# Kernel tuning notes

Hardware: AMD Instinct MI355X
Metric: run time of the kernel (lower is better)

The kernel has to match this reference:

```python
import jax, jax.numpy as jnp
import numpy as np

T, B, H = 2048, 8, 16
KF, VF, KS, VS = 32, 64, 128, 64


def _l2norm(x, eps=1e-6):
    return x / jnp.sqrt(jnp.sum(x * x, axis=-1, keepdims=True) + eps)


def setup_inputs() -> dict:
    key = jax.random.key(0)
    ks = jax.random.split(key, 12)
    # k/q are L2-normalized externally (per E88/E90 kernel contract)
    k_fast = _l2norm(jax.random.normal(ks[0], (T, B, H, KF), jnp.float32))
    q_fast = _l2norm(jax.random.normal(ks[1], (T, B, H, KF), jnp.float32))
    v_fast = jax.random.normal(ks[2], (T, B, H, VF), jnp.float32)
    k_slow = _l2norm(jax.random.normal(ks[3], (T, B, H, KS), jnp.float32))
    q_slow = _l2norm(jax.random.normal(ks[4], (T, B, H, KS), jnp.float32))
    v_slow = jax.random.normal(ks[5], (T, B, H, VS), jnp.float32)
    # decay factors in (0.85, 1.0): typical Mamba2-style per-head scalar decay
    decay_fast = 0.85 + 0.15 * jax.random.uniform(ks[6], (T, B, H), jnp.float32)
    decay_slow = 0.85 + 0.15 * jax.random.uniform(ks[7], (T, B, H), jnp.float32)
    slow_gate = jax.random.uniform(ks[8], (T, B, H), jnp.float32)
    mix_fast = jax.random.uniform(ks[9], (T, B, H), jnp.float32)
    mix_slow = jax.random.uniform(ks[10], (T, B, H), jnp.float32)
    S_fast0 = jnp.zeros((B, H, KF, VF), jnp.float32)
    S_slow0 = jnp.zeros((B, H, KS, VS), jnp.float32)
    return dict(k_fast=k_fast, v_fast=v_fast, q_fast=q_fast, decay_fast=decay_fast,
                k_slow=k_slow, v_slow=v_slow, q_slow=q_slow, decay_slow=decay_slow,
                slow_gate=slow_gate, mix_fast=mix_fast, mix_slow=mix_slow,
                S_fast0=S_fast0, S_slow0=S_slow0, n_heads=H)


def _e90_scan(k_fast, v_fast, q_fast, decay_fast,
              k_slow, v_slow, q_slow, decay_slow,
              slow_gate, mix_fast, mix_slow, S_fast0, S_slow0):
    def step(carry, x):
        S_f, S_s = carry  # [B,H,KF,VF], [B,H,KS,VS]
        kf, vf, qf, df, ksl, vsl, qsl, dsl, g, mf, ms = x
        # fast state: updated every timestep (decay + rank-1 outer product)
        S_f = df[..., None, None] * S_f + kf[..., :, None] * vf[..., None, :]
        # slow state: gated soft update
        S_s_new = dsl[..., None, None] * S_s + ksl[..., :, None] * vsl[..., None, :]
        g_ = g[..., None, None]
        S_s = g_ * S_s_new + (1.0 - g_) * S_s
        out_f = jnp.einsum('bhk,bhkv->bhv', qf, S_f)
        out_s = jnp.einsum('bhk,bhkv->bhv', qsl, S_s)
        out = mf[..., None] * out_f + ms[..., None] * out_s
        return (S_f, S_s), out

    xs = (k_fast, v_fast, q_fast, decay_fast,
          k_slow, v_slow, q_slow, decay_slow,
          slow_gate, mix_fast, mix_slow)
    (S_f_final, S_s_final), output = jax.lax.scan(step, (S_fast0, S_slow0), xs)
    return S_f_final, S_s_final, output  # output: [T,B,H,VF]


def reference(k_fast, v_fast, q_fast, decay_fast, k_slow, v_slow, q_slow,
              decay_slow, slow_gate, mix_fast, mix_slow, S_fast0, S_slow0, n_heads):
    return _e90_scan(k_fast, v_fast, q_fast, decay_fast,
                     k_slow, v_slow, q_slow, decay_slow,
                     slow_gate, mix_fast, mix_slow, S_fast0, S_slow0)
```

## Files before the change

### kernel.cpp

```cpp
#include <hip/hip_runtime.h>

#define T_STEPS 2048
#define BH      128
#define KS_     128
#define VS_     64
#define KF_     32
#define VF_     64
#define LCH     32
#define NC      (T_STEPS / LCH)
#define NTHR    512

typedef __attribute__((ext_vector_type(8))) short short8;
typedef __attribute__((ext_vector_type(16))) float f32x16;

#define MFMA32(a,b,c) __builtin_amdgcn_mfma_f32_32x32x16_bf16((a),(b),(c),0,0,0)
#define CROW(r,hi) (((r)&3) + 8*((r)>>2) + 4*(hi))

__device__ __forceinline__ unsigned short f2b(float x) {
    union { float f; unsigned u; } v; v.f = x;
    unsigned r = v.u + 0x7FFFu + ((v.u >> 16) & 1u);
    return (unsigned short)(r >> 16);
}
__device__ __forceinline__ unsigned cvtpk(float lo, float hi_) {
    unsigned r;
    asm("v_cvt_pk_bf16_f32 %0, %1, %2" : "=v"(r) : "v"(lo), "v"(hi_));
    return r;
}
__device__ __forceinline__ short8 ld8(const unsigned short* p) {
    return *(const short8*)p;
}

__global__ __launch_bounds__(NTHR, 2)
void e90_mfma(const float* __restrict__ k_fast,  const float* __restrict__ v_fast,
              const float* __restrict__ q_fast,  const float* __restrict__ decay_fast,
              const float* __restrict__ k_slow,  const float* __restrict__ v_slow,
              const float* __restrict__ q_slow,  const float* __restrict__ decay_slow,
              const float* __restrict__ slow_gate, const float* __restrict__ mix_fast,
              const float* __restrict__ mix_slow, const float* __restrict__ S_fast0,
              const float* __restrict__ S_slow0, float* __restrict__ dout)
{
    __shared__ __align__(16) unsigned short Qs  [2][LCH][136];
    __shared__ __align__(16) unsigned short Ksl [2][LCH][136];
    __shared__ __align__(16) unsigned short Sbs [2][LCH][136];
    __shared__ __align__(16) unsigned short Psl [2][LCH][40];
    __shared__ __align__(16) unsigned short Pfl [2][LCH][40];
    __shared__ __align__(16) unsigned short Qfl [2][LCH][40];
    __shared__ __align__(16) unsigned short Kfl [2][LCH][40];
    __shared__ __align__(16) unsigned short Sbfl[2][LCH][40];
    __shared__ __align__(16) unsigned short VTs [3][LCH][40];
    __shared__ __align__(16) unsigned short VTf [3][LCH][40];

    const int tid  = threadIdx.x;
    const int bid  = blockIdx.x;
    const int xcd  = bid & 7;
    const int jj   = bid >> 3;
    const int p    = xcd * 16 + (jj >> 1);
    const int v0   = (jj & 1) * 32;
    const int lane = tid & 63;
    const int wid  = tid >> 6;
    const int l31  = lane & 31;
    const int hi   = lane >> 5;
    const int s_   = tid >> 4;
    const int j0_  = (tid & 15) * 2;
    const int k0_  = (tid & 15) * 8;

    float* out_y = dout + BH*KF_*VF_ + BH*KS_*VS_;

    f32x16 Sst, oacc;
#pragma unroll
    for (int r = 0; r < 16; ++r) { Sst[r] = 0.0f; oacc[r] = 0.0f; }
    if (wid < 4) {
#pragma unroll
        for (int r = 0; r < 16; ++r)
            Sst[r] = S_slow0[((size_t)p*KS_ + 32*wid + CROW(r,hi))*VS_ + v0 + l31];
#pragma unroll
        for (int r = 0; r < 16; ++r) Sbs[0][l31][32*wid + CROW(r,hi)] = f2b(Sst[r]);
    } else if (wid == 4) {
#pragma unroll
        for (int r = 0; r < 16; ++r)
            Sst[r] = S_fast0[((size_t)p*KF_ + CROW(r,hi))*VF_ + v0 + l31];
#pragma unroll
        for (int r = 0; r < 16; ++r) Sbfl[0][l31][CROW(r,hi)] = f2b(Sst[r]);
    }

    float4 pKs0, pKs1, pQs0, pQs1;
    float2 pVs, pVf, pKf, pQf;
    float pL0 = 0.f, pL1 = 0.f, pL2 = 0.f;
    float bls = 1.f, blf = 1.f, ib = 1.f, ibf = 1.f, qsc = 0.f, qfc = 0.f, g_s = 0.f;

#define LOADVEC(CIDX) do {                                                     \
    int tc_ = (CIDX); if (tc_ > NC-1) tc_ = NC-1;                              \
    const int tb_ = tc_ * LCH;                                                 \
    const float* bk_ = k_slow + ((size_t)(tb_+s_)*BH + p)*KS_ + k0_;           \
    pKs0 = *(const float4*)bk_;  pKs1 = *(const float4*)(bk_+4);               \
    const float* bq_ = q_slow + ((size_t)(tb_+s_)*BH + p)*KS_ + k0_;           \
    pQs0 = *(const float4*)bq_;  pQs1 = *(const float4*)(bq_+4);               \
    pVs = *(const float2*)(v_slow + ((size_t)(tb_+s_)*BH + p)*VS_ + v0 + j0_); \
    pVf = *(const float2*)(v_fast + ((size_t)(tb_+s_)*BH + p)*VF_ + v0 + j0_); \
    pKf = *(const float2*)(k_fast + ((size_t)(tb_+s_)*BH + p)*KF_ + j0_);      \
    pQf = *(const float2*)(q_fast + ((size_t)(tb_+s_)*BH + p)*KF_ + j0_);      \
    } while (0)

#define LOADSCL(CIDX) do {                                                     \
    int tc_ = (CIDX); if (tc_ > NC-1) tc_ = NC-1;                              \
    const size_t so_ = (size_t)(tc_*LCH + l31)*BH + p;                         \
    pL0 = (hi ? decay_fast : decay_slow)[so_];                                 \
    pL1 = (hi ? mix_fast   : slow_gate )[so_];                                 \
    pL2 = hi ? 0.0f : mix_slow[so_];                                           \
    } while (0)

#define SCAN() do {                                                            \
    float a_ = hi ? pL0 : __builtin_fmaf(pL1, pL0, 1.0f - pL1);                \
    float b_ = a_;                                                             \
    _Pragma("unroll")                                                          \
    for (int d = 1; d < 32; d <<= 1) {                                         \
        float y_ = __shfl_up(b_, d, 32);                                       \
        if (l31 >= d) b_ *= y_;                                                \
    }                                                                          \
    float bs_s = __shfl(b_, s_);                                               \
    float bf_s = __shfl(b_, 32 + s_);                                          \
    bls = __shfl(b_, 31);                                                      \
    blf = __shfl(b_, 63);                                                      \
    g_s = __shfl(pL1, s_);                                                     \
    float mf_s = __shfl(pL1, 32 + s_);                                         \
    float ms_s = __shfl(pL2, s_);                                              \
    ib  = 1.0f / bs_s;                                                         \
    ibf = 1.0f / bf_s;                                                         \
    qsc = ms_s * bs_s;                                                         \
    qfc = mf_s * bf_s;                                                         \
    } while (0)

#define STAGE(J2, J3) do {                                                     \
    uint4 kw, qw;                                                              \
    kw.x = cvtpk(pKs0.x*ib, pKs0.y*ib);  kw.y = cvtpk(pKs0.z*ib, pKs0.w*ib);   \
    kw.z = cvtpk(pKs1.x*ib, pKs1.y*ib);  kw.w = cvtpk(pKs1.z*ib, pKs1.w*ib);   \
    qw.x = cvtpk(pQs0.x*qsc, pQs0.y*qsc); qw.y = cvtpk(pQs0.z*qsc, pQs0.w*qsc);\
    qw.z = cvtpk(pQs1.x*qsc, pQs1.y*qsc); qw.w = cvtpk(pQs1.z*qsc, pQs1.w*qsc);\
    *(uint4*)&Ksl[J2][s_][k0_] = kw;                                           \
    *(uint4*)&Qs [J2][s_][k0_] = qw;                                           \
    float vt0 = g_s*pVs.x, vt1 = g_s*pVs.y;                                    \
    VTs[J3][j0_  ][s_] = f2b(vt0);                                             \
    VTs[J3][j0_+1][s_] = f2b(vt1);                                             \
    VTf[J3][j0_  ][s_] = f2b(pVf.x);                                           \
    VTf[J3][j0_+1][s_] = f2b(pVf.y);                                           \
    unsigned kfp = cvtpk(pKf.x*ibf, pKf.y*ibf);                                \
    *(unsigned*)&Kfl[J2][s_][j0_] = kfp;                                       \
    unsigned qfp = cvtpk(pQf.x*qfc, pQf.y*qfc);                                \
    *(unsigned*)&Qfl[J2][s_][j0_] = qfp;                                       \
    } while (0)

#define YSTORE(CP) do {                                                        \
    const int p2_ = (CP) & 1, p3_ = (CP) % 3;                                  \
    f32x16 o2;                                                                 \
    _Pragma("unroll")                                                          \
    for (int r = 0; r < 16; ++r) o2[r] = 0.0f;                                 \
    const unsigned short* ar = &Psl[p2_][l31][0];                              \
    const unsigned short* br = &VTs[p3_][l31][0];                              \
    oacc = MFMA32(ld8(ar + 8*hi),      ld8(br + 8*hi),      oacc);             \
    oacc = MFMA32(ld8(ar + 16 + 8*hi), ld8(br + 16 + 8*hi), oacc);             \
    const unsigned short* af = &Pfl[p2_][l31][0];                              \
    const unsigned short* bf = &VTf[p3_][l31][0];                              \
    o2 = MFMA32(ld8(af + 8*hi),      ld8(bf + 8*hi),      o2);                 \
    o2 = MFMA32(ld8(af + 16 + 8*hi), ld8(bf + 16 + 8*hi), o2);                 \
    _Pragma("unroll")                                                          \
    for (int r = 0; r < 16; ++r) {                                             \
        int tr = CROW(r,hi);                                                   \
        out_y[((size_t)((CP)*LCH + tr)*BH + p)*VF_ + v0 + l31] = oacc[r] + o2[r]; \
    }                                                                          \
    } while (0)

    LOADVEC(0);
    LOADSCL(0);
    SCAN();
    LOADSCL(1);
    STAGE(0, 0);
    __syncthreads();

    for (int c = 0; c < NC; ++c) {
        const int i2 = c & 1;
        const int i3 = c % 3;

        LOADVEC(c + 1);

        if (wid < 4) {
            short8 a1, a2;
#pragma unroll
            for (int e = 0; e < 8; ++e) {
                a1[e] = (short)Ksl[i2][8*hi + e][32*wid + l31];
                a2[e] = (short)Ksl[i2][16 + 8*hi + e][32*wid + l31];
            }
            const unsigned short* br = &VTs[i3][l31][0];
            Sst = MFMA32(a1, ld8(br + 8*hi),      Sst);
            Sst = MFMA32(a2, ld8(br + 16 + 8*hi), Sst);
#pragma unroll
            for (int r = 0; r < 16; ++r) Sst[r] *= bls;
        } else if (wid == 4) {
            short8 a1, a2;
#pragma unroll
            for (int e = 0; e < 8; ++e) {
                a1[e] = (short)Kfl[i2][8*hi + e][l31];
                a2[e] = (short)Kfl[i2][16 + 8*hi + e][l31];
            }
            const unsigned short* br = &VTf[i3][l31][0];
            Sst = MFMA32(a1, ld8(br + 8*hi),      Sst);
            Sst = MFMA32(a2, ld8(br + 16 + 8*hi), Sst);
#pragma unroll
            for (int r = 0; r < 16; ++r) Sst[r] *= blf;
        } else if (wid == 5) {
            f32x16 p1, p2;
#pragma unroll
            for (int r = 0; r < 16; ++r) { p1[r] = 0.0f; p2[r] = 0.0f; }
            const unsigned short* ar = &Qs [i2][l31][0];
            const unsigned short* br = &Ksl[i2][l31][0];
            const int kb = 8*hi;
#pragma unroll
            for (int st = 0; st < 8; st += 2) {
                p1 = MFMA32(ld8(ar + kb + 16*st),     ld8(br + kb + 16*st),     p1);
                p2 = MFMA32(ld8(ar + kb + 16*(st+1)), ld8(br + kb + 16*(st+1)), p2);
            }
#pragma unroll
            for (int r = 0; r < 16; ++r) {
                int tr = CROW(r,hi);
                Psl[i2][tr][l31] = f2b(tr >= l31 ? p1[r] + p2[r] : 0.0f);
            }
        } else if (wid == 6) {
            f32x16 p1;
#pragma unroll
            for (int r = 0; r < 16; ++r) p1[r] = 0.0f;
            const unsigned short* ar = &Qfl[i2][l31][0];
            const unsigned short* br = &Kfl[i2][l31][0];
            p1 = MFMA32(ld8(ar + 8*hi),      ld8(br + 8*hi),      p1);
            p1 = MFMA32(ld8(ar + 16 + 8*hi), ld8(br + 16 + 8*hi), p1);
#pragma unroll
            for (int r = 0; r < 16; ++r) {
                int tr = CROW(r,hi);
                Pfl[i2][tr][l31] = f2b(tr >= l31 ? p1[r] : 0.0f);
            }
        } else {
            if (c > 0) YSTORE(c - 1);
            f32x16 o1, o2;
#pragma unroll
            for (int r = 0; r < 16; ++r) { o1[r] = 0.0f; o2[r] = 0.0f; }
            const unsigned short* ar = &Qs [i2][l31][0];
            const unsigned short* br = &Sbs[i2][l31][0];
            const int kb = 8*hi;
#pragma unroll
            for (int st = 0; st < 8; st += 2) {
                o1 = MFMA32(ld8(ar + kb + 16*st),     ld8(br + kb + 16*st),     o1);
                o2 = MFMA32(ld8(ar + kb + 16*(st+1)), ld8(br + kb + 16*(st+1)), o2);
            }
            const unsigned short* af = &Qfl [i2][l31][0];
            const unsigned short* bf = &Sbfl[i2][l31][0];
            o1 = MFMA32(ld8(af + 8*hi),      ld8(bf + 8*hi),      o1);
            o2 = MFMA32(ld8(af + 16 + 8*hi), ld8(bf + 16 + 8*hi), o2);
#pragma unroll
            for (int r = 0; r < 16; ++r) oacc[r] = o1[r] + o2[r];
        }

        SCAN();
        LOADSCL(c + 2);

        if (c < NC - 1) {
            const int j2 = (c + 1) & 1;
            const int j3 = (c + 1) % 3;
            if (wid < 4) {
#pragma unroll
                for (int r = 0; r < 16; ++r) Sbs[j2][l31][32*wid + CROW(r,hi)] = f2b(Sst[r]);
            } else if (wid == 4) {
#pragma unroll
                for (int r = 0; r < 16; ++r) Sbfl[j2][l31][CROW(r,hi)] = f2b(Sst[r]);
            }
            STAGE(j2, j3);
        }
        __syncthreads();
    }

    if (wid == 7) {
        YSTORE(NC - 1);
    }
    if (wid < 4) {
#pragma unroll
        for (int r = 0; r < 16; ++r)
            dout[BH*KF_*VF_ + ((size_t)p*KS_ + 32*wid + CROW(r,hi))*VS_ + v0 + l31] = Sst[r];
    } else if (wid == 4) {
#pragma unroll
        for (int r = 0; r < 16; ++r)
            dout[((size_t)p*KF_ + CROW(r,hi))*VF_ + v0 + l31] = Sst[r];
    }
#undef LOADVEC
#undef LOADSCL
#undef SCAN
#undef STAGE
#undef YSTORE
}

extern "C" void kernel_launch(void* const* d_in, const int* in_sizes, int n_in,
                              void* d_out, int out_size, void* d_ws, size_t ws_size,
                              hipStream_t stream)
{
    const float* k_fast     = (const float*)d_in[0];
    const float* v_fast     = (const float*)d_in[1];
    const float* q_fast     = (const float*)d_in[2];
    const float* decay_fast = (const float*)d_in[3];
    const float* k_slow     = (const float*)d_in[4];
    const float* v_slow     = (const float*)d_in[5];
    const float* q_slow     = (const float*)d_in[6];
    const float* decay_slow = (const float*)d_in[7];
    const float* slow_gate  = (const float*)d_in[8];
    const float* mix_fast   = (const float*)d_in[9];
    const float* mix_slow   = (const float*)d_in[10];
    const float* S_fast0    = (const float*)d_in[11];
    const float* S_slow0    = (const float*)d_in[12];
    float* dout = (float*)d_out;

    e90_mfma<<<dim3(256), dim3(NTHR), 0, stream>>>(
        k_fast, v_fast, q_fast, decay_fast,
        k_slow, v_slow, q_slow, decay_slow,
        slow_gate, mix_fast, mix_slow, S_fast0, S_slow0, dout);
}
```

Measured before the change: 186.9 us.

## Split sequence into two halves scanned in parallel with a state-correction kernel

Splits the time axis into two halves so each head/value slice runs two blocks, 512 in total instead of 256. The second half starts from zero state and records per-step cumulative decay scales and its local final state in a workspace. A second fix-up kernel then combines the first half's final state with those scales, adding q·S0 contributions to second-half outputs and correcting the final states. The aim is to double the parallelism of a latency-bound sequential scan, at the cost of an extra launch, workspace traffic, and dropping the multi-stage pipelining of the original loop.

```diff
diff --git a/kernel.cpp b/kernel.cpp
--- a/kernel.cpp
+++ b/kernel.cpp
@@ -7,8 +7,17 @@
 #define KF_     32
 #define VF_     64
 #define LCH     32
+#define NCG     32
 #define NC      (T_STEPS / LCH)
+#define HALF_T  1024
 #define NTHR    512
+#define WSLOT   5120
+#define SCLS_OFF 1310720
+#define SCLF_OFF 1835008
+#define RUN_OFF  2359296
+#define WS_NEEDED_BYTES ((size_t)(RUN_OFF + 512) * 4)
+#define SOFF    (BH*KF_*VF_)
+#define YOFF    (BH*KF_*VF_ + BH*KS_*VS_)
 
 typedef __attribute__((ext_vector_type(8))) short short8;
 typedef __attribute__((ext_vector_type(16))) float f32x16;
@@ -30,8 +39,390 @@
     return *(const short8*)p;
 }
 
+__global__ __launch_bounds__(NTHR, 4)
+void e90_scan(const float* __restrict__ k_fast,  const float* __restrict__ v_fast,
+              const float* __restrict__ q_fast,  const float* __restrict__ decay_fast,
+              const float* __restrict__ k_slow,  const float* __restrict__ v_slow,
+              const float* __restrict__ q_slow,  const float* __restrict__ decay_slow,
+              const float* __restrict__ slow_gate, const float* __restrict__ mix_fast,
+              const float* __restrict__ mix_slow, const float* __restrict__ S_fast0,
+              const float* __restrict__ S_slow0, float* __restrict__ dout,
+              float* __restrict__ dws)
+{
+    __shared__ __align__(16) unsigned short Qs [LCH][136];
+    __shared__ __align__(16) unsigned short Ksl[LCH][136];
+    __shared__ __align__(16) unsigned short Sbs[LCH][136];
+    __shared__ __align__(16) unsigned short Psl[LCH][40];
+    __shared__ __align__(16) unsigned short Pfl[LCH][40];
+    __shared__ __align__(16) unsigned short Qfl[LCH][40];
+    __shared__ __align__(16) unsigned short Kfl[LCH][40];
+    __shared__ __align__(16) unsigned short Sbfl[LCH][40];
+    __shared__ __align__(16) unsigned short VTs[2][LCH][40];
+    __shared__ __align__(16) unsigned short VTf[2][LCH][40];
+
+    const int tid  = threadIdx.x;
+    const int bid  = blockIdx.x;
+    const int xcd  = bid & 7;
+    const int q8   = bid >> 3;
+    const int p    = xcd * 16 + (q8 >> 2);
+    const int vh   = (q8 >> 1) & 1;
+    const int v0   = vh * 32;
+    const int th   = q8 & 1;
+    const int tgb  = th * HALF_T;
+    const int slot = p * 2 + vh;
+    const int lane = tid & 63;
+    const int wid  = tid >> 6;
+    const int l31  = lane & 31;
+    const int hi   = lane >> 5;
+    const int s_   = tid >> 4;
+    const int j0_  = (tid & 15) * 2;
+    const int k0_  = (tid & 15) * 8;
+
+    float* out_y = dout + YOFF;
+
+    f32x16 Sst, oacc;
+#pragma unroll
+    for (int r = 0; r < 16; ++r) { Sst[r] = 0.0f; oacc[r] = 0.0f; }
+    if (th == 0) {
+        if (wid < 4) {
+#pragma unroll
+            for (int r = 0; r < 16; ++r)
+                Sst[r] = S_slow0[((size_t)p*KS_ + 32*wid + CROW(r,hi))*VS_ + v0 + l31];
+        } else if (wid == 4) {
+#pragma unroll
+            for (int r = 0; r < 16; ++r)
+                Sst[r] = S_fast0[((size_t)p*KF_ + CROW(r,hi))*VF_ + v0 + l31];
+        }
+    }
+    if (wid < 4) {
+#pragma unroll
+        for (int r = 0; r < 16; ++r) Sbs[l31][32*wid + CROW(r,hi)] = f2b(Sst[r]);
+    } else if (wid == 4) {
+#pragma unroll
+        for (int r = 0; r < 16; ++r) Sbfl[l31][CROW(r,hi)] = f2b(Sst[r]);
+    }
+
+    float4 pKs0, pKs1, pQs0, pQs1;
+    float2 pVs, pVf, pKf, pQf;
+    float pL0 = 0.f, pL1 = 0.f, pL2 = 0.f;
+
+#define LOADCHUNK(CIDX) do {                                                   \
+    int tc_ = (CIDX); if (tc_ > NCG-1) tc_ = NCG-1;                            \
+    const int tb_ = tgb + tc_ * LCH;                                           \
+    const float* bk_ = k_slow + ((size_t)(tb_+s_)*BH + p)*KS_ + k0_;           \
+    pKs0 = *(const float4*)bk_;  pKs1 = *(const float4*)(bk_+4);               \
+    const float* bq_ = q_slow + ((size_t)(tb_+s_)*BH + p)*KS_ + k0_;           \
+    pQs0 = *(const float4*)bq_;  pQs1 = *(const float4*)(bq_+4);               \
+    pVs = *(const float2*)(v_slow + ((size_t)(tb_+s_)*BH + p)*VS_ + v0 + j0_); \
+    pVf = *(const float2*)(v_fast + ((size_t)(tb_+s_)*BH + p)*VF_ + v0 + j0_); \
+    pKf = *(const float2*)(k_fast + ((size_t)(tb_+s_)*BH + p)*KF_ + j0_);      \
+    pQf = *(const float2*)(q_fast + ((size_t)(tb_+s_)*BH + p)*KF_ + j0_);      \
+    const size_t so_ = (size_t)(tb_ + l31)*BH + p;                             \
+    pL0 = (hi ? decay_fast : decay_slow)[so_];                                 \
+    pL1 = (hi ? mix_fast   : slow_gate )[so_];                                 \
+    pL2 = hi ? 0.0f : mix_slow[so_];                                           \
+    } while (0)
+
+    LOADCHUNK(0);
+
+    float bls = 1.f, blf = 1.f, ib = 1.f, ibf = 1.f, qsc = 0.f, qfc = 0.f, g_s = 0.f;
+    float runAcc = 1.0f;
+
+    for (int c = 0; c < NCG; ++c) {
+        const int cb = c & 1;
+        if (c > 0) {
+            if (wid < 4) {
+#pragma unroll
+                for (int r = 0; r < 16; ++r) Sbs[l31][32*wid + CROW(r,hi)] = f2b(Sst[r]);
+            } else if (wid == 4) {
+#pragma unroll
+                for (int r = 0; r < 16; ++r) Sbfl[l31][CROW(r,hi)] = f2b(Sst[r]);
+            } else if (wid == 7) {
+                const int pb = cb ^ 1;
+                f32x16 o2;
+#pragma unroll
+                for (int r = 0; r < 16; ++r) o2[r] = 0.0f;
+                const unsigned short* ar = &Psl[l31][0];
+                const unsigned short* br = &VTs[pb][l31][0];
+                oacc = MFMA32(ld8(ar + 8*hi),      ld8(br + 8*hi),      oacc);
+                oacc = MFMA32(ld8(ar + 16 + 8*hi), ld8(br + 16 + 8*hi), oacc);
+                const unsigned short* af = &Pfl[l31][0];
+                const unsigned short* bf = &VTf[pb][l31][0];
+                o2 = MFMA32(ld8(af + 8*hi),      ld8(bf + 8*hi),      o2);
+                o2 = MFMA32(ld8(af + 16 + 8*hi), ld8(bf + 16 + 8*hi), o2);
+#pragma unroll
+                for (int r = 0; r < 16; ++r) {
+                    int tr = CROW(r,hi);
+                    out_y[((size_t)(tgb + (c-1)*LCH + tr)*BH + p)*VF_ + v0 + l31] = oacc[r] + o2[r];
+                }
+            }
+        }
+        {
+            float a = hi ? pL0 : __builtin_fmaf(pL1, pL0, 1.0f - pL1);
+            float b = a;
+#pragma unroll
+            for (int d = 1; d < 32; d <<= 1) {
+                float y = __shfl_up(b, d, 32);
+                if (l31 >= d) b *= y;
+            }
+            if (th == 1 && wid == 0) {
+                float sc = (hi ? pL1 : pL2) * b * runAcc;
+                float* wsp = dws + (hi ? SCLF_OFF : SCLS_OFF) + (size_t)slot*HALF_T + c*LCH + l31;
+                *wsp = sc;
+            }
+            float bs_s = __shfl(b, s_);
+            float bf_s = __shfl(b, 32 + s_);
+            bls = __shfl(b, 31);
+            blf = __shfl(b, 63);
+            g_s = __shfl(pL1, s_);
+            float mf_s = __shfl(pL1, 32 + s_);
+            float ms_s = __shfl(pL2, s_);
+            ib  = 1.0f / bs_s;
+            ibf = 1.0f / bf_s;
+            qsc = ms_s * bs_s;
+            qfc = mf_s * bf_s;
+            runAcc *= (hi ? blf : bls);
+        }
+        {
+            uint4 kw, qw;
+            kw.x = cvtpk(pKs0.x*ib, pKs0.y*ib);  kw.y = cvtpk(pKs0.z*ib, pKs0.w*ib);
+            kw.z = cvtpk(pKs1.x*ib, pKs1.y*ib);  kw.w = cvtpk(pKs1.z*ib, pKs1.w*ib);
+            qw.x = cvtpk(pQs0.x*qsc, pQs0.y*qsc); qw.y = cvtpk(pQs0.z*qsc, pQs0.w*qsc);
+            qw.z = cvtpk(pQs1.x*qsc, pQs1.y*qsc); qw.w = cvtpk(pQs1.z*qsc, pQs1.w*qsc);
+            *(uint4*)&Ksl[s_][k0_] = kw;
+            *(uint4*)&Qs [s_][k0_] = qw;
+
+            float vt0 = g_s*pVs.x, vt1 = g_s*pVs.y;
+            VTs[cb][j0_  ][s_] = f2b(vt0);
+            VTs[cb][j0_+1][s_] = f2b(vt1);
+            VTf[cb][j0_  ][s_] = f2b(pVf.x);
+            VTf[cb][j0_+1][s_] = f2b(pVf.y);
+            unsigned kfp = cvtpk(pKf.x*ibf, pKf.y*ibf);
+            *(unsigned*)&Kfl[s_][j0_] = kfp;
+            unsigned qfp = cvtpk(pQf.x*qfc, pQf.y*qfc);
+            *(unsigned*)&Qfl[s_][j0_] = qfp;
+        }
+        __syncthreads();
+
+        LOADCHUNK(c + 1);
+
+        if (wid < 4) {
+            short8 a1, a2;
+#pragma unroll
+            for (int e = 0; e < 8; ++e) {
+                a1[e] = (short)Ksl[8*hi + e][32*wid + l31];
+                a2[e] = (short)Ksl[16 + 8*hi + e][32*wid + l31];
+            }
+            const unsigned short* br = &VTs[cb][l31][0];
+            Sst = MFMA32(a1, ld8(br + 8*hi),      Sst);
+            Sst = MFMA32(a2, ld8(br + 16 + 8*hi), Sst);
+#pragma unroll
+            for (int r = 0; r < 16; ++r) Sst[r] *= bls;
+        } else if (wid == 4) {
+            short8 a1, a2;
+#pragma unroll
+            for (int e = 0; e < 8; ++e) {
+                a1[e] = (short)Kfl[8*hi + e][l31];
+                a2[e] = (short)Kfl[16 + 8*hi + e][l31];
+            }
+            const unsigned short* br = &VTf[cb][l31][0];
+            Sst = MFMA32(a1, ld8(br + 8*hi),      Sst);
+            Sst = MFMA32(a2, ld8(br + 16 + 8*hi), Sst);
+#pragma unroll
+            for (int r = 0; r < 16; ++r) Sst[r] *= blf;
+        } else if (wid == 5) {
+            f32x16 p1, p2;
+#pragma unroll
+            for (int r = 0; r < 16; ++r) { p1[r] = 0.0f; p2[r] = 0.0f; }
+            const unsigned short* ar = &Qs [l31][0];
+            const unsigned short* br = &Ksl[l31][0];
+            const int kb = 8*hi;
+#pragma unroll
+            for (int st = 0; st < 8; st += 2) {
+                p1 = MFMA32(ld8(ar + kb + 16*st),     ld8(br + kb + 16*st),     p1);
+                p2 = MFMA32(ld8(ar + kb + 16*(st+1)), ld8(br + kb + 16*(st+1)), p2);
+            }
+#pragma unroll
+            for (int r = 0; r < 16; ++r) {
+                int tr = CROW(r,hi);
+                Psl[tr][l31] = f2b(tr >= l31 ? p1[r] + p2[r] : 0.0f);
+            }
+        } else if (wid == 6) {
+            f32x16 p1;
+#pragma unroll
+            for (int r = 0; r < 16; ++r) p1[r] = 0.0f;
+            const unsigned short* ar = &Qfl[l31][0];
+            const unsigned short* br = &Kfl[l31][0];
+            p1 = MFMA32(ld8(ar + 8*hi),      ld8(br + 8*hi),      p1);
+            p1 = MFMA32(ld8(ar + 16 + 8*hi), ld8(br + 16 + 8*hi), p1);
+#pragma unroll
+            for (int r = 0; r < 16; ++r) {
+                int tr = CROW(r,hi);
+                Pfl[tr][l31] = f2b(tr >= l31 ? p1[r] : 0.0f);
+            }
+        } else {
+            f32x16 o1, o2;
+#pragma unroll
+            for (int r = 0; r < 16; ++r) { o1[r] = 0.0f; o2[r] = 0.0f; }
+            const unsigned short* ar = &Qs [l31][0];
+            const unsigned short* br = &Sbs[l31][0];
+            const int kb = 8*hi;
+#pragma unroll
+            for (int st = 0; st < 8; st += 2) {
+                o1 = MFMA32(ld8(ar + kb + 16*st),     ld8(br + kb + 16*st),     o1);
+                o2 = MFMA32(ld8(ar + kb + 16*(st+1)), ld8(br + kb + 16*(st+1)), o2);
+            }
+            const unsigned short* af = &Qfl [l31][0];
+            const unsigned short* bf = &Sbfl[l31][0];
+            o1 = MFMA32(ld8(af + 8*hi),      ld8(bf + 8*hi),      o1);
+            o2 = MFMA32(ld8(af + 16 + 8*hi), ld8(bf + 16 + 8*hi), o2);
+#pragma unroll
+            for (int r = 0; r < 16; ++r) oacc[r] = o1[r] + o2[r];
+        }
+        __syncthreads();
+    }
+
+    if (wid == 7) {
+        const int pb = (NCG - 1) & 1;
+        f32x16 o2;
+#pragma unroll
+        for (int r = 0; r < 16; ++r) o2[r] = 0.0f;
+        const unsigned short* ar = &Psl[l31][0];
+        const unsigned short* br = &VTs[pb][l31][0];
+        oacc = MFMA32(ld8(ar + 8*hi),      ld8(br + 8*hi),      oacc);
+        oacc = MFMA32(ld8(ar + 16 + 8*hi), ld8(br + 16 + 8*hi), oacc);
+        const unsigned short* af = &Pfl[l31][0];
+        const unsigned short* bf = &VTf[pb][l31][0];
+        o2 = MFMA32(ld8(af + 8*hi),      ld8(bf + 8*hi),      o2);
+        o2 = MFMA32(ld8(af + 16 + 8*hi), ld8(bf + 16 + 8*hi), o2);
+#pragma unroll
+        for (int r = 0; r < 16; ++r) {
+            int tr = CROW(r,hi);
+            out_y[((size_t)(tgb + (NCG-1)*LCH + tr)*BH + p)*VF_ + v0 + l31] = oacc[r] + o2[r];
+        }
+    }
+
+    if (th == 0) {
+        if (wid < 4) {
+#pragma unroll
+            for (int r = 0; r < 16; ++r)
+                dout[SOFF + ((size_t)p*KS_ + 32*wid + CROW(r,hi))*VS_ + v0 + l31] = Sst[r];
+        } else if (wid == 4) {
+#pragma unroll
+            for (int r = 0; r < 16; ++r)
+                dout[((size_t)p*KF_ + CROW(r,hi))*VF_ + v0 + l31] = Sst[r];
+        }
+    } else {
+        if (wid < 4) {
+#pragma unroll
+            for (int r = 0; r < 16; ++r)
+                dws[(size_t)slot*WSLOT + (32*wid + CROW(r,hi))*32 + l31] = Sst[r];
+        } else if (wid == 4) {
+#pragma unroll
+            for (int r = 0; r < 16; ++r)
+                dws[(size_t)slot*WSLOT + (128 + CROW(r,hi))*32 + l31] = Sst[r];
+        }
+        if (wid == 0 && lane == 0)  dws[RUN_OFF + slot*2 + 0] = runAcc;
+        if (wid == 0 && lane == 32) dws[RUN_OFF + slot*2 + 1] = runAcc;
+    }
+#undef LOADCHUNK
+}
+
 __global__ __launch_bounds__(NTHR, 2)
-void e90_mfma(const float* __restrict__ k_fast,  const float* __restrict__ v_fast,
+void e90_fix(const float* __restrict__ q_fast, const float* __restrict__ q_slow,
+             const float* __restrict__ dws, float* __restrict__ dout)
+{
+    __shared__ __align__(16) unsigned short SbS[32][136];
+    __shared__ __align__(16) unsigned short SbF[32][40];
+
+    const int tid  = threadIdx.x;
+    const int bid  = blockIdx.x;
+    const int xcd  = bid & 7;
+    const int jj   = bid >> 3;
+    const int p    = xcd * 16 + (jj >> 1);
+    const int vh   = jj & 1;
+    const int v0   = vh * 32;
+    const int slot = p * 2 + vh;
+    const int lane = tid & 63;
+    const int w8   = tid >> 6;
+    const int l31  = lane & 31;
+    const int hi   = lane >> 5;
+
+    float* out_y = dout + YOFF;
+
+    for (int i = tid; i < 128 * 32; i += NTHR) {
+        int k = i >> 5, v = i & 31;
+        SbS[v][k] = f2b(dout[SOFF + ((size_t)p*KS_ + k)*VS_ + v0 + v]);
+    }
+    for (int i = tid; i < 32 * 32; i += NTHR) {
+        int k = i >> 5, v = i & 31;
+        SbF[v][k] = f2b(dout[((size_t)p*KF_ + k)*VF_ + v0 + v]);
+    }
+    __syncthreads();
+
+    {
+        const float runS = dws[RUN_OFF + slot*2 + 0];
+        const float runF = dws[RUN_OFF + slot*2 + 1];
+        for (int i = tid; i < WSLOT; i += NTHR) {
+            int k = i >> 5, v = i & 31;
+            float st = dws[(size_t)slot*WSLOT + i];
+            if (k < 128) {
+                size_t o = SOFF + ((size_t)p*KS_ + k)*VS_ + v0 + v;
+                dout[o] = runS * dout[o] + st;
+            } else {
+                size_t o = ((size_t)p*KF_ + (k - 128))*VF_ + v0 + v;
+                dout[o] = runF * dout[o] + st;
+            }
+        }
+    }
+
+#pragma unroll 1
+    for (int j = 0; j < 4; ++j) {
+        const int cc = w8 * 4 + j;
+        const int t0 = HALF_T + cc * LCH;
+        const float sS = dws[SCLS_OFF + (size_t)slot*HALF_T + cc*LCH + l31];
+        const float sF = dws[SCLF_OFF + (size_t)slot*HALF_T + cc*LCH + l31];
+        const size_t so = (size_t)(t0 + l31) * BH + p;
+        f32x16 c1, c2;
+#pragma unroll
+        for (int r = 0; r < 16; ++r) { c1[r] = 0.0f; c2[r] = 0.0f; }
+#pragma unroll
+        for (int st = 0; st < 8; ++st) {
+            const float* qp = q_slow + so*KS_ + 16*st + 8*hi;
+            float4 x = *(const float4*)qp;
+            float4 y = *(const float4*)(qp + 4);
+            union { unsigned u[4]; short8 s; } fr;
+            fr.u[0] = cvtpk(x.x*sS, x.y*sS);
+            fr.u[1] = cvtpk(x.z*sS, x.w*sS);
+            fr.u[2] = cvtpk(y.x*sS, y.y*sS);
+            fr.u[3] = cvtpk(y.z*sS, y.w*sS);
+            if (st & 1) c2 = MFMA32(fr.s, ld8(&SbS[l31][16*st + 8*hi]), c2);
+            else        c1 = MFMA32(fr.s, ld8(&SbS[l31][16*st + 8*hi]), c1);
+        }
+#pragma unroll
+        for (int st = 0; st < 2; ++st) {
+            const float* qp = q_fast + so*KF_ + 16*st + 8*hi;
+            float4 x = *(const float4*)qp;
+            float4 y = *(const float4*)(qp + 4);
+            union { unsigned u[4]; short8 s; } fr;
+            fr.u[0] = cvtpk(x.x*sF, x.y*sF);
+            fr.u[1] = cvtpk(x.z*sF, x.w*sF);
+            fr.u[2] = cvtpk(y.x*sF, y.y*sF);
+            fr.u[3] = cvtpk(y.z*sF, y.w*sF);
+            if (st & 1) c2 = MFMA32(fr.s, ld8(&SbF[l31][16*st + 8*hi]), c2);
+            else        c1 = MFMA32(fr.s, ld8(&SbF[l31][16*st + 8*hi]), c1);
+        }
+#pragma unroll
+        for (int r = 0; r < 16; ++r) {
+            int tr = CROW(r,hi);
+            size_t o = ((size_t)(t0 + tr)*BH + p)*VF_ + v0 + l31;
+            out_y[o] += c1[r] + c2[r];
+        }
+    }
+}
+
+__global__ __launch_bounds__(NTHR, 2)
+void e90_mono(const float* __restrict__ k_fast,  const float* __restrict__ v_fast,
               const float* __restrict__ q_fast,  const float* __restrict__ decay_fast,
               const float* __restrict__ k_slow,  const float* __restrict__ v_slow,
               const float* __restrict__ q_slow,  const float* __restrict__ decay_slow,
@@ -64,7 +455,7 @@
     const int j0_  = (tid & 15) * 2;
     const int k0_  = (tid & 15) * 8;
 
-    float* out_y = dout + BH*KF_*VF_ + BH*KS_*VS_;
+    float* out_y = dout + YOFF;
 
     f32x16 Sst, oacc;
 #pragma unroll
@@ -179,7 +570,6 @@
     for (int c = 0; c < NC; ++c) {
         const int i2 = c & 1;
         const int i3 = c % 3;
-
         LOADVEC(c + 1);
 
         if (wid < 4) {
@@ -281,7 +671,7 @@
     if (wid < 4) {
 #pragma unroll
         for (int r = 0; r < 16; ++r)
-            dout[BH*KF_*VF_ + ((size_t)p*KS_ + 32*wid + CROW(r,hi))*VS_ + v0 + l31] = Sst[r];
+            dout[SOFF + ((size_t)p*KS_ + 32*wid + CROW(r,hi))*VS_ + v0 + l31] = Sst[r];
     } else if (wid == 4) {
 #pragma unroll
         for (int r = 0; r < 16; ++r)
@@ -312,9 +702,18 @@
     const float* S_fast0    = (const float*)d_in[11];
     const float* S_slow0    = (const float*)d_in[12];
     float* dout = (float*)d_out;
-
-    e90_mfma<<<dim3(256), dim3(NTHR), 0, stream>>>(
-        k_fast, v_fast, q_fast, decay_fast,
-        k_slow, v_slow, q_slow, decay_slow,
-        slow_gate, mix_fast, mix_slow, S_fast0, S_slow0, dout);
+    float* dws  = (float*)d_ws;
+
+    if (ws_size >= WS_NEEDED_BYTES) {
+        e90_scan<<<dim3(512), dim3(NTHR), 0, stream>>>(
+            k_fast, v_fast, q_fast, decay_fast,
+            k_slow, v_slow, q_slow, decay_slow,
+            slow_gate, mix_fast, mix_slow, S_fast0, S_slow0, dout, dws);
+        e90_fix<<<dim3(256), dim3(NTHR), 0, stream>>>(q_fast, q_slow, dws, dout);
+    } else {
+        e90_mono<<<dim3(256), dim3(NTHR), 0, stream>>>(
+            k_fast, v_fast, q_fast, decay_fast,
+            k_slow, v_slow, q_slow, decay_slow,
+            slow_gate, mix_fast, mix_slow, S_fast0, S_slow0, dout);
+    }
 }
```

Result: slower. 302.7 us (+61.9%).
